# Performance work log

Hardware: AMD Instinct MI355X
Metric: run time of the kernel (lower is better)

The kernel has to match this reference:

```python
import jax, jax.numpy as jnp
import numpy as np
from jax import lax

N = 100000
G = 256          # voxel grid extent per axis
MULT = 8
C_HID = 32 * MULT  # 256
K3 = 27


def setup_inputs() -> dict:
    key = jax.random.key(0)
    k_feat, k1, k2, k3, k4 = jax.random.split(key, 5)
    # unique voxel coordinates in a G^3 grid (sparse tensors have no duplicate coords)
    rng = np.random.default_rng(0)
    lin = rng.choice(G * G * G, size=N, replace=False)
    coords = np.stack([lin // (G * G), (lin // G) % G, lin % G], axis=1).astype(np.int32)
    feats = jax.random.normal(k_feat, (N, 2), dtype=jnp.float32)
    def w(k, cin, cout):
        return jax.random.normal(k, (K3, cin, cout), dtype=jnp.float32) / np.sqrt(K3 * cin)
    return {
        "coords": jnp.asarray(coords),
        "feats": feats,
        "W1": w(k1, 2, C_HID),
        "W2": w(k2, C_HID, C_HID),
        "W3": w(k3, C_HID, C_HID),
        "W4": w(k4, C_HID, 2),
    }


def _neighbor_map(coords):
    """Kernel map for a 3x3x3 stride-1 sparse conv: for each of 27 offsets and each
    point i, the index j of the point at coords[i]+offset (and a validity mask).
    Built once and shared by all four layers (stride=1 preserves coordinates)."""
    S = G + 2  # pad linearization base so offsets in {-1,0,1} never wrap
    c = coords.astype(jnp.int32) + 1
    keys = (c[:, 0] * S + c[:, 1]) * S + c[:, 2]            # [N]
    order = jnp.argsort(keys)
    skeys = keys[order]
    offs = jnp.array([[dx, dy, dz] for dx in (-1, 0, 1)
                      for dy in (-1, 0, 1) for dz in (-1, 0, 1)], dtype=jnp.int32)  # [27,3]
    nc = c[None, :, :] + offs[:, None, :]                    # [27,N,3]
    qk = (nc[..., 0] * S + nc[..., 1]) * S + nc[..., 2]      # [27,N]
    pos = jnp.clip(jnp.searchsorted(skeys, qk), 0, N - 1)
    valid = skeys[pos] == qk                                 # [27,N]
    idx = order[pos]                                         # [27,N]
    return idx, valid


def _sparse_conv(feats, W, idx, valid):
    """gather -> GEMM -> accumulate, scanned over the 27 kernel offsets."""
    out0 = jnp.zeros((feats.shape[0], W.shape[-1]), feats.dtype)
    def step(acc, kv):
        i, v, w = kv
        g = jnp.where(v[:, None], feats[i], 0.0)   # [N,Cin] gathered neighbor feats
        return acc + g @ w, None
    out, _ = lax.scan(step, out0, (idx, valid, W))
    return out


def reference(coords, feats, W1, W2, W3, W4):
    idx, valid = _neighbor_map(coords)
    x = _sparse_conv(feats, W1, idx, valid)
    x = _sparse_conv(x, W2, idx, valid)
    x = _sparse_conv(x, W3, idx, valid)
    x = _sparse_conv(x, W4, idx, valid)
    return x
```

## Files before the change

kernel.cpp:

```cpp
#include <hip/hip_runtime.h>

#define HASH_BITS 19
#define HASH_SIZE (1u << HASH_BITS)
#define HASH_MASK (HASH_SIZE - 1)
#define EMPTY64 0xFFFFFFFFFFFFFFFFull
#define CH 256
#define PCH 32
#define NREP 8
#define NSEG (27 * NREP)
#define SEGCAP 4096
#define BM_WORDS 536704

typedef __attribute__((ext_vector_type(8))) short short8;
typedef __attribute__((ext_vector_type(4))) float floatx4;
typedef unsigned long long ull;

__device__ __forceinline__ unsigned cvt_pk_bf16(float a, float b) {
    unsigned r;
    asm("v_cvt_pk_bf16_f32 %0, %1, %2" : "=v"(r) : "v"(a), "v"(b));
    return r;
}

__device__ inline void split8_pack(const float* xa, uint4& hv, uint4& lv) {
#pragma unroll
    for (int p = 0; p < 4; ++p) {
        unsigned hp = cvt_pk_bf16(xa[2 * p], xa[2 * p + 1]);
        float h0 = __uint_as_float(hp << 16);
        float h1 = __uint_as_float(hp & 0xFFFF0000u);
        unsigned lp = cvt_pk_bf16(xa[2 * p] - h0, xa[2 * p + 1] - h1);
        ((unsigned*)&hv)[p] = hp;
        ((unsigned*)&lv)[p] = lp;
    }
}

__global__ void hash_insert_k(const int* __restrict__ coords, int n,
                              ull* __restrict__ tbl, unsigned* __restrict__ keys,
                              unsigned* __restrict__ bm) {
    int i = blockIdx.x * blockDim.x + threadIdx.x;
    if (i >= n) return;
    unsigned cx = (unsigned)(coords[3 * i + 0] + 1);
    unsigned cy = (unsigned)(coords[3 * i + 1] + 1);
    unsigned cz = (unsigned)(coords[3 * i + 2] + 1);
    unsigned key = (cx * 258u + cy) * 258u + cz;
    keys[i] = key;
    atomicOr(&bm[key >> 5], 1u << (key & 31));
    ull e = ((ull)key << 32) | (unsigned)i;
    unsigned h = (key * 2654435761u) & HASH_MASK;
    while (true) {
        ull prev = atomicCAS(&tbl[h], EMPTY64, e);
        if (prev == EMPTY64) return;
        h = (h + 1) & HASH_MASK;
    }
}

__global__ void neighbor_bm_k(const unsigned* __restrict__ keys, int n,
                              const unsigned* __restrict__ bm,
                              const ull* __restrict__ tbl,
                              int2* __restrict__ buckets, int* __restrict__ kcnt) {
    int t = blockIdx.x * blockDim.x + threadIdx.x;
    if (t >= n * 9) return;
    int rep = blockIdx.x & (NREP - 1);
    int i = t / 9, r = t - i * 9;
    unsigned key = keys[i];
    int base = (int)key + ((r / 3 - 1) * 258 + (r % 3 - 1)) * 258;
    unsigned bA = base - 1, bB = base, bC = base + 1;
    unsigned hit0 = (bm[bA >> 5] >> (bA & 31)) & 1u;
    unsigned hit1 = (bm[bB >> 5] >> (bB & 31)) & 1u;
    unsigned hit2 = (bm[bC >> 5] >> (bC & 31)) & 1u;
#pragma unroll
    for (int dz = -1; dz <= 1; ++dz) {
        if (r == 4 && dz == 0) continue;
        unsigned hit = dz < 0 ? hit0 : (dz == 0 ? hit1 : hit2);
        if (!hit) continue;
        unsigned nk = (unsigned)(base + dz);
        unsigned h = (nk * 2654435761u) & HASH_MASK;
        int j = -1;
        while (true) {
            ull e = tbl[h];
            if ((unsigned)(e >> 32) == nk) { j = (int)(e & 0xFFFFFFFFu); break; }
            if (e == EMPTY64) break;
            h = (h + 1) & HASH_MASK;
        }
        if (j >= 0) {
            int kk = 3 * r + dz + 1;
            int seg = kk * NREP + rep;
            int pos = atomicAdd(&kcnt[seg * 16], 1);
            buckets[(size_t)seg * SEGCAP + pos] = make_int2(i, j);
        }
    }
}

__global__ void chunk_desc_k(const int* __restrict__ kcnt,
                             int2* __restrict__ desc, int* __restrict__ nchunks) {
    __shared__ int cnts[NSEG];
    __shared__ int offs[NSEG + 1];
    int t = threadIdx.x;
    if (t < NSEG) cnts[t] = kcnt[t * 16];
    __syncthreads();
    if (t == 0) {
        int acc = 0;
        for (int s = 0; s < NSEG; ++s) { offs[s] = acc; acc += (cnts[s] + PCH - 1) / PCH; }
        offs[NSEG] = acc;
        *nchunks = acc;
    }
    __syncthreads();
    if (t < NSEG) {
        int cnt = cnts[t];
        int o = offs[t];
        int k = t / NREP;
        for (int c = 0; c * PCH < cnt; ++c) {
            int len = min(PCH, cnt - c * PCH);
            desc[o + c] = make_int2(t * SEGCAP + c * PCH, (k << 8) | len);
        }
    }
}

__global__ void prep_w_all_k(const float* __restrict__ W, unsigned short* __restrict__ Whi,
                             unsigned short* __restrict__ Wlo) {
    int t = blockIdx.x * 256 + threadIdx.x;
    if (t >= 27 * 8 * 256) return;
    int cout = t & 255, kk = (t >> 8) & 7, k = t >> 11;
    int nt = cout >> 4, lc = cout & 15;
    const float* src = W + (size_t)k * 65536 + (size_t)kk * 32 * 256 + cout;
    size_t dbase = (((size_t)(k * 8 + kk) * 16 + nt) * 64 + lc) * 8;
#pragma unroll
    for (int kg = 0; kg < 4; ++kg) {
        float xa[8];
#pragma unroll
        for (int j = 0; j < 8; ++j) xa[j] = src[(size_t)(kg * 8 + j) * 256];
        uint4 hv, lv;
        split8_pack(xa, hv, lv);
        *(uint4*)(Whi + dbase + (size_t)kg * 16 * 8) = hv;
        *(uint4*)(Wlo + dbase + (size_t)kg * 16 * 8) = lv;
    }
}

__global__ void dense1_k(const float* __restrict__ x, const float* __restrict__ Wc,
                         float* __restrict__ out, int n) {
    int t = blockIdx.x * blockDim.x + threadIdx.x;
    if (t >= n * CH) return;
    int i = t >> 8, co = t & 255;
    float2 xv = *reinterpret_cast<const float2*>(x + 2 * i);
    out[t] = fmaf(xv.x, Wc[co], xv.y * Wc[CH + co]);
}

__global__ void sparse1b_k(const float* __restrict__ feats, const float* __restrict__ W1,
                           float* __restrict__ out, const int2* __restrict__ buckets,
                           const int2* __restrict__ desc, const int* __restrict__ nchunks) {
    __shared__ float xs[PCH][2];
    __shared__ int ii[PCH];
    int nc = *nchunks;
    int t = threadIdx.x;
    for (int m = blockIdx.x; m < nc; m += gridDim.x) {
        int2 d = desc[m];
        int k = d.y >> 8, len = d.y & 255;
        if (t < PCH) {
            if (t < len) {
                int2 pr = buckets[d.x + t];
                ii[t] = pr.x;
                xs[t][0] = feats[2 * pr.y];
                xs[t][1] = feats[2 * pr.y + 1];
            } else {
                ii[t] = -1;
                xs[t][0] = 0.f; xs[t][1] = 0.f;
            }
        }
        __syncthreads();
        const float* Wk = W1 + (size_t)k * 2 * CH;
        float w0 = Wk[t], w1 = Wk[CH + t];
#pragma unroll
        for (int p = 0; p < PCH; ++p) {
            int i = ii[p];
            if (i >= 0) atomicAdd(&out[(size_t)i * CH + t], fmaf(xs[p][0], w0, xs[p][1] * w1));
        }
        __syncthreads();
    }
}

__global__ __launch_bounds__(256, 3) void dense_mid_mfma_k(
        const float* __restrict__ x,
        const unsigned short* __restrict__ Whi,
        const unsigned short* __restrict__ Wlo,
        float* __restrict__ out, int n) {
    __shared__ unsigned short AsH[3][2048], AsL[3][2048];
    int t = threadIdx.x;
    int wid = t >> 6, lane = t & 63;
    int i0 = blockIdx.x * 64;

    floatx4 acc[4][4];
#pragma unroll
    for (int a = 0; a < 4; ++a)
#pragma unroll
        for (int b = 0; b < 4; ++b) acc[a][b] = floatx4{0.f, 0.f, 0.f, 0.f};

    int row = ((t >> 6) << 4) + (t & 15);
    int kg = (t >> 4) & 3;
    float sok = (i0 + row < n) ? 1.f : 0.f;
    const float* sp = x + (size_t)min(i0 + row, n - 1) * CH + kg * 8;

    floatx4 ra0, ra1;
    short8 Bh[2][4], Bl[2][4];

    auto loadB = [&](int kk, int b) {
#pragma unroll
        for (int q = 0; q < 4; ++q) {
            size_t off = (((size_t)kk * 16 + wid * 4 + q) * 64 + lane) * 8;
            Bh[b][q] = *(const short8*)&Whi[off];
            Bl[b][q] = *(const short8*)&Wlo[off];
        }
    };
    auto loadA = [&](int kk) {
        ra0 = *(const floatx4*)(sp + kk * 32);
        ra1 = *(const floatx4*)(sp + kk * 32 + 4);
    };
    auto writeA = [&](int bi) {
        float xa[8];
        xa[0] = ra0.x * sok; xa[1] = ra0.y * sok; xa[2] = ra0.z * sok; xa[3] = ra0.w * sok;
        xa[4] = ra1.x * sok; xa[5] = ra1.y * sok; xa[6] = ra1.z * sok; xa[7] = ra1.w * sok;
        uint4 hv, lv;
        split8_pack(xa, hv, lv);
        *(uint4*)&AsH[bi][t * 8] = hv;
        *(uint4*)&AsL[bi][t * 8] = lv;
    };
    auto compute = [&](int bi, int b) {
#pragma unroll
        for (int mt = 0; mt < 4; ++mt) {
            short8 ah = *(const short8*)&AsH[bi][(mt * 64 + lane) * 8];
            short8 al = *(const short8*)&AsL[bi][(mt * 64 + lane) * 8];
#pragma unroll
            for (int q = 0; q < 4; ++q) {
                acc[mt][q] = __builtin_amdgcn_mfma_f32_16x16x32_bf16(ah, Bh[b][q], acc[mt][q], 0, 0, 0);
                acc[mt][q] = __builtin_amdgcn_mfma_f32_16x16x32_bf16(al, Bh[b][q], acc[mt][q], 0, 0, 0);
                acc[mt][q] = __builtin_amdgcn_mfma_f32_16x16x32_bf16(ah, Bl[b][q], acc[mt][q], 0, 0, 0);
            }
        }
    };

    loadB(0, 0);
    loadA(0); writeA(0);
    loadA(1); writeA(1);
    __syncthreads();

#pragma unroll
    for (int kk = 0; kk < 8; ++kk) {
        if (kk < 7) loadB(kk + 1, (kk + 1) & 1);
        if (kk < 6) loadA(kk + 2);
        compute(kk % 3, kk & 1);
        if (kk < 6) writeA((kk + 2) % 3);
        __syncthreads();
    }

    int r0 = (lane >> 4) * 4, c0 = lane & 15;
#pragma unroll
    for (int mt = 0; mt < 4; ++mt)
#pragma unroll
        for (int r = 0; r < 4; ++r) {
            int orow = i0 + mt * 16 + r0 + r;
            if (orow < n) {
#pragma unroll
                for (int q = 0; q < 4; ++q)
                    out[(size_t)orow * CH + wid * 64 + q * 16 + c0] = acc[mt][q][r];
            }
        }
}

__global__ __launch_bounds__(256) void sparse_mid_mfma_k(
        const float* __restrict__ x,
        const unsigned short* __restrict__ Whi,
        const unsigned short* __restrict__ Wlo,
        float* __restrict__ out, const int2* __restrict__ buckets,
        const int2* __restrict__ desc, const int* __restrict__ nchunks) {
    __shared__ unsigned short As_hi[8192];
    __shared__ unsigned short As_lo[8192];
    __shared__ int ii[PCH];
    int nc = *nchunks;
    int t = threadIdx.x;
    int wid = t >> 6, lane = t & 63;
    int r = t >> 3, kk0 = t & 7;
    int mt_s = r >> 4, rl = r & 15;
    for (int m = blockIdx.x; m < nc; m += gridDim.x) {
        int2 d = desc[m];
        int k = d.y >> 8, len = d.y & 255;
        if (r < len) {
            int2 pr = buckets[d.x + r];
            if (kk0 == 0) ii[r] = pr.x;
            const float* src = x + (size_t)pr.y * CH + kk0 * 32;
#pragma unroll
            for (int kg = 0; kg < 4; ++kg) {
                float xa[8];
                floatx4 v0 = *(const floatx4*)(src + kg * 8);
                floatx4 v1 = *(const floatx4*)(src + kg * 8 + 4);
                xa[0] = v0.x; xa[1] = v0.y; xa[2] = v0.z; xa[3] = v0.w;
                xa[4] = v1.x; xa[5] = v1.y; xa[6] = v1.z; xa[7] = v1.w;
                uint4 hv, lv;
                split8_pack(xa, hv, lv);
                int ab = ((kk0 * 2 + mt_s) * 64 + kg * 16 + rl) * 8;
                *(uint4*)&As_hi[ab] = hv;
                *(uint4*)&As_lo[ab] = lv;
            }
        } else {
            if (kk0 == 0) ii[r] = -1;
            uint4 z = {0, 0, 0, 0};
#pragma unroll
            for (int kg = 0; kg < 4; ++kg) {
                int ab = ((kk0 * 2 + mt_s) * 64 + kg * 16 + rl) * 8;
                *(uint4*)&As_hi[ab] = z;
                *(uint4*)&As_lo[ab] = z;
            }
        }
        __syncthreads();
        floatx4 acc[2][4];
#pragma unroll
        for (int a = 0; a < 2; ++a)
#pragma unroll
            for (int b = 0; b < 4; ++b) acc[a][b] = floatx4{0.f, 0.f, 0.f, 0.f};
        for (int kk = 0; kk < 8; ++kk) {
            short8 ah0 = *(const short8*)&As_hi[((kk * 2 + 0) * 64 + lane) * 8];
            short8 al0 = *(const short8*)&As_lo[((kk * 2 + 0) * 64 + lane) * 8];
            short8 ah1 = *(const short8*)&As_hi[((kk * 2 + 1) * 64 + lane) * 8];
            short8 al1 = *(const short8*)&As_lo[((kk * 2 + 1) * 64 + lane) * 8];
#pragma unroll
            for (int q = 0; q < 4; ++q) {
                int nt = wid * 4 + q;
                size_t off = (((size_t)(k * 8 + kk) * 16 + nt) * 64 + lane) * 8;
                short8 bh = *(const short8*)&Whi[off];
                short8 bl = *(const short8*)&Wlo[off];
                acc[0][q] = __builtin_amdgcn_mfma_f32_16x16x32_bf16(ah0, bh, acc[0][q], 0, 0, 0);
                acc[0][q] = __builtin_amdgcn_mfma_f32_16x16x32_bf16(al0, bh, acc[0][q], 0, 0, 0);
                acc[0][q] = __builtin_amdgcn_mfma_f32_16x16x32_bf16(ah0, bl, acc[0][q], 0, 0, 0);
                acc[1][q] = __builtin_amdgcn_mfma_f32_16x16x32_bf16(ah1, bh, acc[1][q], 0, 0, 0);
                acc[1][q] = __builtin_amdgcn_mfma_f32_16x16x32_bf16(al1, bh, acc[1][q], 0, 0, 0);
                acc[1][q] = __builtin_amdgcn_mfma_f32_16x16x32_bf16(ah1, bl, acc[1][q], 0, 0, 0);
            }
        }
        int r0 = (lane >> 4) * 4, c0 = lane & 15;
#pragma unroll
        for (int mt = 0; mt < 2; ++mt)
#pragma unroll
            for (int rr = 0; rr < 4; ++rr) {
                int row = mt * 16 + r0 + rr;
                int i = ii[row];
                if (i >= 0) {
#pragma unroll
                    for (int q = 0; q < 4; ++q)
                        atomicAdd(&out[(size_t)i * CH + wid * 64 + q * 16 + c0], acc[mt][q][rr]);
                }
            }
        __syncthreads();
    }
}

__device__ inline float wave_sum(float v) {
    for (int off = 32; off; off >>= 1) v += __shfl_xor(v, off);
    return v;
}

__global__ void dense4_k(const float* __restrict__ x, const float* __restrict__ Wc,
                         float* __restrict__ out, int n) {
    int wid = threadIdx.x >> 6, lane = threadIdx.x & 63;
    int i = blockIdx.x * 4 + wid;
    if (i >= n) return;
    floatx4 xv = *reinterpret_cast<const floatx4*>(x + (size_t)i * CH + lane * 4);
    floatx4 w0 = *reinterpret_cast<const floatx4*>(Wc + lane * 8);
    floatx4 w1 = *reinterpret_cast<const floatx4*>(Wc + lane * 8 + 4);
    float a0 = xv.x * w0.x + xv.y * w0.z + xv.z * w1.x + xv.w * w1.z;
    float a1 = xv.x * w0.y + xv.y * w0.w + xv.z * w1.y + xv.w * w1.w;
    a0 = wave_sum(a0);
    a1 = wave_sum(a1);
    if (lane == 0) { out[2 * i] = a0; out[2 * i + 1] = a1; }
}

__global__ void sparse4b_k(const float* __restrict__ x, const float* __restrict__ W4,
                           float* __restrict__ out, const int2* __restrict__ buckets,
                           const int2* __restrict__ desc, const int* __restrict__ nchunks) {
    int nc = *nchunks;
    int wid = threadIdx.x >> 6, lane = threadIdx.x & 63;
    for (int m = blockIdx.x; m < nc; m += gridDim.x) {
        int2 d = desc[m];
        int k = d.y >> 8, len = d.y & 255;
        const float* Wk = W4 + (size_t)k * CH * 2;
        floatx4 w0 = *reinterpret_cast<const floatx4*>(Wk + lane * 8);
        floatx4 w1 = *reinterpret_cast<const floatx4*>(Wk + lane * 8 + 4);
        for (int p = wid; p < len; p += 4) {
            int2 pr = buckets[d.x + p];
            floatx4 xv = *reinterpret_cast<const floatx4*>(x + (size_t)pr.y * CH + lane * 4);
            float a0 = xv.x * w0.x + xv.y * w0.z + xv.z * w1.x + xv.w * w1.z;
            float a1 = xv.x * w0.y + xv.y * w0.w + xv.z * w1.y + xv.w * w1.w;
            a0 = wave_sum(a0);
            a1 = wave_sum(a1);
            if (lane == 0) {
                atomicAdd(&out[2 * pr.x], a0);
                atomicAdd(&out[2 * pr.x + 1], a1);
            }
        }
    }
}

extern "C" void kernel_launch(void* const* d_in, const int* in_sizes, int n_in,
                              void* d_out, int out_size, void* d_ws, size_t ws_size,
                              hipStream_t stream) {
    const int* coords = (const int*)d_in[0];
    const float* feats = (const float*)d_in[1];
    const float* W1 = (const float*)d_in[2];
    const float* W2 = (const float*)d_in[3];
    const float* W3 = (const float*)d_in[4];
    const float* W4 = (const float*)d_in[5];
    float* out = (float*)d_out;
    int n = in_sizes[0] / 3;

    char* ws = (char*)d_ws;
    auto alloc = [&](size_t bytes) -> void* {
        void* p = (void*)ws;
        ws += (bytes + 255) & ~(size_t)255;
        return p;
    };
    ull* tbl = (ull*)alloc((size_t)HASH_SIZE * 8);
    unsigned* bm = (unsigned*)alloc((size_t)BM_WORDS * 4);
    unsigned* keys = (unsigned*)alloc((size_t)n * 4);
    int* kcnt = (int*)alloc((size_t)NSEG * 16 * 4);
    int* nchunks = (int*)alloc(4);
    int ndesc = NSEG * (SEGCAP / PCH);
    int2* desc = (int2*)alloc(sizeof(int2) * (size_t)ndesc);
    int2* buckets = (int2*)alloc(sizeof(int2) * (size_t)NSEG * SEGCAP);
    unsigned short* Whi2 = (unsigned short*)alloc((size_t)27 * 65536 * 2);
    unsigned short* Wlo2 = (unsigned short*)alloc((size_t)27 * 65536 * 2);
    unsigned short* Whi3 = (unsigned short*)alloc((size_t)27 * 65536 * 2);
    unsigned short* Wlo3 = (unsigned short*)alloc((size_t)27 * 65536 * 2);
    float* x1 = (float*)alloc((size_t)n * CH * 4);
    float* x2 = (float*)alloc((size_t)n * CH * 4);

    hipMemsetAsync(tbl, 0xFF, (size_t)HASH_SIZE * 8, stream);
    hipMemsetAsync(bm, 0, (size_t)BM_WORDS * 4, stream);
    hipMemsetAsync(kcnt, 0, (size_t)NSEG * 16 * 4, stream);

    hash_insert_k<<<(n + 255) / 256, 256, 0, stream>>>(coords, n, tbl, keys, bm);
    neighbor_bm_k<<<(n * 9 + 255) / 256, 256, 0, stream>>>(keys, n, bm, tbl, buckets, kcnt);
    chunk_desc_k<<<1, 256, 0, stream>>>(kcnt, desc, nchunks);
    prep_w_all_k<<<(27 * 8 * 256) / 256, 256, 0, stream>>>(W2, Whi2, Wlo2);
    prep_w_all_k<<<(27 * 8 * 256) / 256, 256, 0, stream>>>(W3, Whi3, Wlo3);

    int mtiles = (n + 63) / 64;

    dense1_k<<<(n * CH + 255) / 256, 256, 0, stream>>>(feats, W1 + 13 * 2 * CH, x1, n);
    sparse1b_k<<<1024, 256, 0, stream>>>(feats, W1, x1, buckets, desc, nchunks);

    dense_mid_mfma_k<<<mtiles, 256, 0, stream>>>(x1, Whi2 + (size_t)13 * 65536,
                                                 Wlo2 + (size_t)13 * 65536, x2, n);
    sparse_mid_mfma_k<<<512, 256, 0, stream>>>(x1, Whi2, Wlo2, x2, buckets, desc, nchunks);

    dense_mid_mfma_k<<<mtiles, 256, 0, stream>>>(x2, Whi3 + (size_t)13 * 65536,
                                                 Wlo3 + (size_t)13 * 65536, x1, n);
    sparse_mid_mfma_k<<<512, 256, 0, stream>>>(x2, Whi3, Wlo3, x1, buckets, desc, nchunks);

    dense4_k<<<(n + 3) / 4, 256, 0, stream>>>(x1, W4 + 13 * CH * 2, out, n);
    sparse4b_k<<<512, 256, 0, stream>>>(x1, W4, out, buckets, desc, nchunks);
}
```

Measured before the change: 304.1 us.

## Stage full A tile in LDS, prefetch B in sparse conv, merge launches

The dense center-tap GEMM now converts and stores all eight K-slices of the A tile into shared memory up front, so the main loop has no per-step barriers. This costs 64KB of LDS per block and drops the launch-bounds occupancy hint. The sparse MFMA kernel now double-buffers its weight fragment loads one K-step ahead instead of loading them just before each MFMA. Separately, the two weight-prep launches are merged into one, and the two memsets become one by placing kcnt right after the bitmap.

After: 301.6 us. Within noise of the previous version (-0.8%).

```diff
diff --git a/kernel.cpp b/kernel.cpp
--- a/kernel.cpp
+++ b/kernel.cpp
@@ -115,11 +115,17 @@
     }
 }
 
-__global__ void prep_w_all_k(const float* __restrict__ W, unsigned short* __restrict__ Whi,
-                             unsigned short* __restrict__ Wlo) {
+__global__ void prep_w_all_k(const float* __restrict__ W2, const float* __restrict__ W3,
+                             unsigned short* __restrict__ Whi2, unsigned short* __restrict__ Wlo2,
+                             unsigned short* __restrict__ Whi3, unsigned short* __restrict__ Wlo3) {
     int t = blockIdx.x * 256 + threadIdx.x;
-    if (t >= 27 * 8 * 256) return;
-    int cout = t & 255, kk = (t >> 8) & 7, k = t >> 11;
+    const int HALF = 27 * 8 * 256;
+    if (t >= 2 * HALF) return;
+    const float* W = (t < HALF) ? W2 : W3;
+    unsigned short* Whi = (t < HALF) ? Whi2 : Whi3;
+    unsigned short* Wlo = (t < HALF) ? Wlo2 : Wlo3;
+    int tt = (t < HALF) ? t : t - HALF;
+    int cout = tt & 255, kk = (tt >> 8) & 7, k = tt >> 11;
     int nt = cout >> 4, lc = cout & 15;
     const float* src = W + (size_t)k * 65536 + (size_t)kk * 32 * 256 + cout;
     size_t dbase = (((size_t)(k * 8 + kk) * 16 + nt) * 64 + lc) * 8;
@@ -177,30 +183,42 @@
     }
 }
 
-__global__ __launch_bounds__(256, 3) void dense_mid_mfma_k(
+__global__ __launch_bounds__(256) void dense_mid_mfma_k(
         const float* __restrict__ x,
         const unsigned short* __restrict__ Whi,
         const unsigned short* __restrict__ Wlo,
         float* __restrict__ out, int n) {
-    __shared__ unsigned short AsH[3][2048], AsL[3][2048];
+    __shared__ unsigned short AsH[8][2048];
+    __shared__ unsigned short AsL[8][2048];
     int t = threadIdx.x;
     int wid = t >> 6, lane = t & 63;
     int i0 = blockIdx.x * 64;
-
-    floatx4 acc[4][4];
-#pragma unroll
-    for (int a = 0; a < 4; ++a)
-#pragma unroll
-        for (int b = 0; b < 4; ++b) acc[a][b] = floatx4{0.f, 0.f, 0.f, 0.f};
 
     int row = ((t >> 6) << 4) + (t & 15);
     int kg = (t >> 4) & 3;
     float sok = (i0 + row < n) ? 1.f : 0.f;
     const float* sp = x + (size_t)min(i0 + row, n - 1) * CH + kg * 8;
-
-    floatx4 ra0, ra1;
+#pragma unroll
+    for (int kk = 0; kk < 8; ++kk) {
+        floatx4 v0 = *(const floatx4*)(sp + kk * 32);
+        floatx4 v1 = *(const floatx4*)(sp + kk * 32 + 4);
+        float xa[8];
+        xa[0] = v0.x * sok; xa[1] = v0.y * sok; xa[2] = v0.z * sok; xa[3] = v0.w * sok;
+        xa[4] = v1.x * sok; xa[5] = v1.y * sok; xa[6] = v1.z * sok; xa[7] = v1.w * sok;
+        uint4 hv, lv;
+        split8_pack(xa, hv, lv);
+        *(uint4*)&AsH[kk][t * 8] = hv;
+        *(uint4*)&AsL[kk][t * 8] = lv;
+    }
+    __syncthreads();
+
+    floatx4 acc[4][4];
+#pragma unroll
+    for (int a = 0; a < 4; ++a)
+#pragma unroll
+        for (int b = 0; b < 4; ++b) acc[a][b] = floatx4{0.f, 0.f, 0.f, 0.f};
+
     short8 Bh[2][4], Bl[2][4];
-
     auto loadB = [&](int kk, int b) {
 #pragma unroll
         for (int q = 0; q < 4; ++q) {
@@ -209,24 +227,16 @@
             Bl[b][q] = *(const short8*)&Wlo[off];
         }
     };
-    auto loadA = [&](int kk) {
-        ra0 = *(const floatx4*)(sp + kk * 32);
-        ra1 = *(const floatx4*)(sp + kk * 32 + 4);
-    };
-    auto writeA = [&](int bi) {
-        float xa[8];
-        xa[0] = ra0.x * sok; xa[1] = ra0.y * sok; xa[2] = ra0.z * sok; xa[3] = ra0.w * sok;
-        xa[4] = ra1.x * sok; xa[5] = ra1.y * sok; xa[6] = ra1.z * sok; xa[7] = ra1.w * sok;
-        uint4 hv, lv;
-        split8_pack(xa, hv, lv);
-        *(uint4*)&AsH[bi][t * 8] = hv;
-        *(uint4*)&AsL[bi][t * 8] = lv;
-    };
-    auto compute = [&](int bi, int b) {
+
+    loadB(0, 0);
+#pragma unroll
+    for (int kk = 0; kk < 8; ++kk) {
+        if (kk < 7) loadB(kk + 1, (kk + 1) & 1);
+        int b = kk & 1;
 #pragma unroll
         for (int mt = 0; mt < 4; ++mt) {
-            short8 ah = *(const short8*)&AsH[bi][(mt * 64 + lane) * 8];
-            short8 al = *(const short8*)&AsL[bi][(mt * 64 + lane) * 8];
+            short8 ah = *(const short8*)&AsH[kk][(mt * 64 + lane) * 8];
+            short8 al = *(const short8*)&AsL[kk][(mt * 64 + lane) * 8];
 #pragma unroll
             for (int q = 0; q < 4; ++q) {
                 acc[mt][q] = __builtin_amdgcn_mfma_f32_16x16x32_bf16(ah, Bh[b][q], acc[mt][q], 0, 0, 0);
@@ -234,20 +244,6 @@
                 acc[mt][q] = __builtin_amdgcn_mfma_f32_16x16x32_bf16(ah, Bl[b][q], acc[mt][q], 0, 0, 0);
             }
         }
-    };
-
-    loadB(0, 0);
-    loadA(0); writeA(0);
-    loadA(1); writeA(1);
-    __syncthreads();
-
-#pragma unroll
-    for (int kk = 0; kk < 8; ++kk) {
-        if (kk < 7) loadB(kk + 1, (kk + 1) & 1);
-        if (kk < 6) loadA(kk + 2);
-        compute(kk % 3, kk & 1);
-        if (kk < 6) writeA((kk + 2) % 3);
-        __syncthreads();
     }
 
     int r0 = (lane >> 4) * 4, c0 = lane & 15;
@@ -314,23 +310,33 @@
         for (int a = 0; a < 2; ++a)
 #pragma unroll
             for (int b = 0; b < 4; ++b) acc[a][b] = floatx4{0.f, 0.f, 0.f, 0.f};
+
+        short8 bh[2][4], bl[2][4];
+        auto loadBs = [&](int kk, int b) {
+#pragma unroll
+            for (int q = 0; q < 4; ++q) {
+                size_t off = (((size_t)(k * 8 + kk) * 16 + wid * 4 + q) * 64 + lane) * 8;
+                bh[b][q] = *(const short8*)&Whi[off];
+                bl[b][q] = *(const short8*)&Wlo[off];
+            }
+        };
+        loadBs(0, 0);
+#pragma unroll
         for (int kk = 0; kk < 8; ++kk) {
+            if (kk < 7) loadBs(kk + 1, (kk + 1) & 1);
+            int b = kk & 1;
             short8 ah0 = *(const short8*)&As_hi[((kk * 2 + 0) * 64 + lane) * 8];
             short8 al0 = *(const short8*)&As_lo[((kk * 2 + 0) * 64 + lane) * 8];
             short8 ah1 = *(const short8*)&As_hi[((kk * 2 + 1) * 64 + lane) * 8];
             short8 al1 = *(const short8*)&As_lo[((kk * 2 + 1) * 64 + lane) * 8];
 #pragma unroll
             for (int q = 0; q < 4; ++q) {
-                int nt = wid * 4 + q;
-                size_t off = (((size_t)(k * 8 + kk) * 16 + nt) * 64 + lane) * 8;
-                short8 bh = *(const short8*)&Whi[off];
-                short8 bl = *(const short8*)&Wlo[off];
-                acc[0][q] = __builtin_amdgcn_mfma_f32_16x16x32_bf16(ah0, bh, acc[0][q], 0, 0, 0);
-                acc[0][q] = __builtin_amdgcn_mfma_f32_16x16x32_bf16(al0, bh, acc[0][q], 0, 0, 0);
-                acc[0][q] = __builtin_amdgcn_mfma_f32_16x16x32_bf16(ah0, bl, acc[0][q], 0, 0, 0);
-                acc[1][q] = __builtin_amdgcn_mfma_f32_16x16x32_bf16(ah1, bh, acc[1][q], 0, 0, 0);
-                acc[1][q] = __builtin_amdgcn_mfma_f32_16x16x32_bf16(al1, bh, acc[1][q], 0, 0, 0);
-                acc[1][q] = __builtin_amdgcn_mfma_f32_16x16x32_bf16(ah1, bl, acc[1][q], 0, 0, 0);
+                acc[0][q] = __builtin_amdgcn_mfma_f32_16x16x32_bf16(ah0, bh[b][q], acc[0][q], 0, 0, 0);
+                acc[0][q] = __builtin_amdgcn_mfma_f32_16x16x32_bf16(al0, bh[b][q], acc[0][q], 0, 0, 0);
+                acc[0][q] = __builtin_amdgcn_mfma_f32_16x16x32_bf16(ah0, bl[b][q], acc[0][q], 0, 0, 0);
+                acc[1][q] = __builtin_amdgcn_mfma_f32_16x16x32_bf16(ah1, bh[b][q], acc[1][q], 0, 0, 0);
+                acc[1][q] = __builtin_amdgcn_mfma_f32_16x16x32_bf16(al1, bh[b][q], acc[1][q], 0, 0, 0);
+                acc[1][q] = __builtin_amdgcn_mfma_f32_16x16x32_bf16(ah1, bl[b][q], acc[1][q], 0, 0, 0);
             }
         }
         int r0 = (lane >> 4) * 4, c0 = lane & 15;
@@ -338,8 +344,8 @@
         for (int mt = 0; mt < 2; ++mt)
 #pragma unroll
             for (int rr = 0; rr < 4; ++rr) {
-                int row = mt * 16 + r0 + rr;
-                int i = ii[row];
+                int orow = mt * 16 + r0 + rr;
+                int i = ii[orow];
                 if (i >= 0) {
 #pragma unroll
                     for (int q = 0; q < 4; ++q)
@@ -416,8 +422,8 @@
     };
     ull* tbl = (ull*)alloc((size_t)HASH_SIZE * 8);
     unsigned* bm = (unsigned*)alloc((size_t)BM_WORDS * 4);
+    int* kcnt = (int*)alloc((size_t)NSEG * 16 * 4);
     unsigned* keys = (unsigned*)alloc((size_t)n * 4);
-    int* kcnt = (int*)alloc((size_t)NSEG * 16 * 4);
     int* nchunks = (int*)alloc(4);
     int ndesc = NSEG * (SEGCAP / PCH);
     int2* desc = (int2*)alloc(sizeof(int2) * (size_t)ndesc);
@@ -430,14 +436,12 @@
     float* x2 = (float*)alloc((size_t)n * CH * 4);
 
     hipMemsetAsync(tbl, 0xFF, (size_t)HASH_SIZE * 8, stream);
-    hipMemsetAsync(bm, 0, (size_t)BM_WORDS * 4, stream);
-    hipMemsetAsync(kcnt, 0, (size_t)NSEG * 16 * 4, stream);
+    hipMemsetAsync(bm, 0, (size_t)BM_WORDS * 4 + (size_t)NSEG * 16 * 4, stream);
 
     hash_insert_k<<<(n + 255) / 256, 256, 0, stream>>>(coords, n, tbl, keys, bm);
     neighbor_bm_k<<<(n * 9 + 255) / 256, 256, 0, stream>>>(keys, n, bm, tbl, buckets, kcnt);
     chunk_desc_k<<<1, 256, 0, stream>>>(kcnt, desc, nchunks);
-    prep_w_all_k<<<(27 * 8 * 256) / 256, 256, 0, stream>>>(W2, Whi2, Wlo2);
-    prep_w_all_k<<<(27 * 8 * 256) / 256, 256, 0, stream>>>(W3, Whi3, Wlo3);
+    prep_w_all_k<<<(2 * 27 * 8 * 256) / 256, 256, 0, stream>>>(W2, W3, Whi2, Wlo2, Whi3, Wlo3);
 
     int mtiles = (n + 63) / 64;
 
```
